# Optimization experiments

Hardware: AMD Instinct MI355X
Metric: run time of the kernel (lower is better)

The kernel has to match this reference:

```python
import jax, jax.numpy as jnp
import numpy as np

HIDDEN = 1024
SEQ = 32768


def setup_inputs() -> dict:
    key = jax.random.key(0)
    k1, k2, k3, k4 = jax.random.split(key, 4)
    scale = 1.0 / np.sqrt(HIDDEN)
    return {
        "hidden": jax.random.normal(k1, (HIDDEN,), dtype=jnp.float32),
        "encoder_outputs": jax.random.normal(k2, (SEQ, HIDDEN), dtype=jnp.float32),
        "W": jax.random.normal(k3, (HIDDEN, HIDDEN), dtype=jnp.float32) * scale,
        "b": jax.random.normal(k4, (HIDDEN,), dtype=jnp.float32) * scale,
    }


def reference(hidden, encoder_outputs, W, b):
    # method == 'general': energy_i = Linear(enc_i); score_i = hidden . energy_i
    # Batched: energies = (enc @ W.T + b) @ hidden   -> [S]
    proj = jnp.einsum("sh,oh->so", encoder_outputs, W) + b  # [S, H]
    energies = proj @ hidden                                  # [S]
    attn = jax.nn.softmax(energies, axis=-1)                  # softmax over seq
    return attn[None, None, :]                                # [1, 1, S]
```

## Files before the change

### kernel.cpp

```cpp
#include <hip/hip_runtime.h>
#include <math.h>

#define H 1024
#define S 32768

__global__ void matvec_partial_kernel(const float* __restrict__ W,
                                      const float* __restrict__ hidden,
                                      float* __restrict__ vpart) {
    const int t = threadIdx.x;
    const int b = blockIdx.x;
    const int h4 = t * 4;
    float4 acc = make_float4(0.f, 0.f, 0.f, 0.f);
    const int o0 = b * 16;
#pragma unroll
    for (int i = 0; i < 16; ++i) {
        const int o = o0 + i;
        const float hv = hidden[o];
        const float4 w = *reinterpret_cast<const float4*>(&W[(size_t)o * H + h4]);
        acc.x += hv * w.x;
        acc.y += hv * w.y;
        acc.z += hv * w.z;
        acc.w += hv * w.w;
    }
    *reinterpret_cast<float4*>(&vpart[(size_t)b * H + h4]) = acc;
}

__global__ void matvec_reduce_kernel(const float* __restrict__ vpart,
                                     float* __restrict__ v) {
    const int t = threadIdx.x;
    const int h4 = t * 4;
    float4 acc = make_float4(0.f, 0.f, 0.f, 0.f);
#pragma unroll 8
    for (int b = 0; b < 64; ++b) {
        const float4 p = *reinterpret_cast<const float4*>(&vpart[(size_t)b * H + h4]);
        acc.x += p.x;
        acc.y += p.y;
        acc.z += p.z;
        acc.w += p.w;
    }
    *reinterpret_cast<float4*>(&v[h4]) = acc;
}

__global__ void energies_kernel(const float* __restrict__ enc,
                                const float* __restrict__ v,
                                float* __restrict__ energies) {
    const int wave = threadIdx.x >> 6;
    const int lane = threadIdx.x & 63;
    const int s = blockIdx.x * 4 + wave;
    const float* row = enc + (size_t)s * H;
    float acc = 0.f;
#pragma unroll
    for (int j = 0; j < 4; ++j) {
        const int idx = j * 256 + lane * 4;
        const float4 e  = *reinterpret_cast<const float4*>(&row[idx]);
        const float4 vv = *reinterpret_cast<const float4*>(&v[idx]);
        acc += e.x * vv.x + e.y * vv.y + e.z * vv.z + e.w * vv.w;
    }
#pragma unroll
    for (int off = 32; off > 0; off >>= 1)
        acc += __shfl_down(acc, off, 64);
    if (lane == 0) energies[s] = acc;
}

__global__ void softmax_kernel(const float* __restrict__ energies,
                               float* __restrict__ out) {
    __shared__ float red[16];
    const int t = threadIdx.x;
    const int lane = t & 63;
    const int wid = t >> 6;

    float m = -INFINITY;
    for (int i = t; i < S; i += 1024) m = fmaxf(m, energies[i]);
#pragma unroll
    for (int off = 32; off > 0; off >>= 1)
        m = fmaxf(m, __shfl_down(m, off, 64));
    if (lane == 0) red[wid] = m;
    __syncthreads();
    if (t < 16) {
        float mm = red[t];
#pragma unroll
        for (int off = 8; off > 0; off >>= 1)
            mm = fmaxf(mm, __shfl_down(mm, off, 16));
        if (t == 0) red[0] = mm;
    }
    __syncthreads();
    m = red[0];
    __syncthreads();

    float ssum = 0.f;
    for (int i = t; i < S; i += 1024) ssum += __expf(energies[i] - m);
#pragma unroll
    for (int off = 32; off > 0; off >>= 1)
        ssum += __shfl_down(ssum, off, 64);
    if (lane == 0) red[wid] = ssum;
    __syncthreads();
    if (t < 16) {
        float sm = red[t];
#pragma unroll
        for (int off = 8; off > 0; off >>= 1)
            sm += __shfl_down(sm, off, 16);
        if (t == 0) red[0] = sm;
    }
    __syncthreads();
    const float inv = 1.0f / red[0];

    for (int i = t; i < S; i += 1024)
        out[i] = __expf(energies[i] - m) * inv;
}

extern "C" void kernel_launch(void* const* d_in, const int* in_sizes, int n_in,
                              void* d_out, int out_size, void* d_ws, size_t ws_size,
                              hipStream_t stream) {
    const float* hidden = (const float*)d_in[0];
    const float* enc    = (const float*)d_in[1];
    const float* W      = (const float*)d_in[2];
    float* out = (float*)d_out;

    float* vpart    = (float*)d_ws;
    float* v        = vpart + 64 * H;
    float* energies = v + H;

    matvec_partial_kernel<<<64, 256, 0, stream>>>(W, hidden, vpart);
    matvec_reduce_kernel<<<1, 256, 0, stream>>>(vpart, v);
    energies_kernel<<<S / 4, 256, 0, stream>>>(enc, v, energies);
    softmax_kernel<<<1, 1024, 0, stream>>>(energies, out);
}
```

Baseline: 218.2 us.

## Fuse per-block online-softmax max/sum into energies kernel, 4 rows per wave

The energies kernel now has each wave compute four rows, keeping v in registers, and each block emits a partial max and rescaled exp-sum (online softmax). The single-block finalize kernel then merges 2048 partials instead of scanning all 32768 energies twice, leaving only one pass to normalize. This shrinks the serial single-block work at the cost of extra exps in the energies kernel and fewer blocks (2048) for the memory-bound scan.

```diff
diff --git a/kernel.cpp b/kernel.cpp
--- a/kernel.cpp
+++ b/kernel.cpp
@@ -43,69 +43,103 @@
 
 __global__ void energies_kernel(const float* __restrict__ enc,
                                 const float* __restrict__ v,
-                                float* __restrict__ energies) {
+                                float* __restrict__ energies,
+                                float* __restrict__ mpart,
+                                float* __restrict__ spart) {
     const int wave = threadIdx.x >> 6;
     const int lane = threadIdx.x & 63;
-    const int s = blockIdx.x * 4 + wave;
-    const float* row = enc + (size_t)s * H;
-    float acc = 0.f;
+    const int gwave = blockIdx.x * 4 + wave;
+    const int s0 = gwave * 4;
+
+    float4 vv[4];
 #pragma unroll
-    for (int j = 0; j < 4; ++j) {
-        const int idx = j * 256 + lane * 4;
-        const float4 e  = *reinterpret_cast<const float4*>(&row[idx]);
-        const float4 vv = *reinterpret_cast<const float4*>(&v[idx]);
-        acc += e.x * vv.x + e.y * vv.y + e.z * vv.z + e.w * vv.w;
+    for (int j = 0; j < 4; ++j)
+        vv[j] = *reinterpret_cast<const float4*>(&v[j * 256 + lane * 4]);
+
+    float e[4];
+#pragma unroll
+    for (int r = 0; r < 4; ++r) {
+        const float* row = enc + (size_t)(s0 + r) * H;
+        float acc = 0.f;
+#pragma unroll
+        for (int j = 0; j < 4; ++j) {
+            const float4 ev = *reinterpret_cast<const float4*>(&row[j * 256 + lane * 4]);
+            acc += ev.x * vv[j].x + ev.y * vv[j].y + ev.z * vv[j].z + ev.w * vv[j].w;
+        }
+#pragma unroll
+        for (int off = 32; off > 0; off >>= 1)
+            acc += __shfl_xor(acc, off, 64);
+        e[r] = acc;
     }
-#pragma unroll
-    for (int off = 32; off > 0; off >>= 1)
-        acc += __shfl_down(acc, off, 64);
-    if (lane == 0) energies[s] = acc;
+
+    if (lane == 0) {
+        energies[s0 + 0] = e[0];
+        energies[s0 + 1] = e[1];
+        energies[s0 + 2] = e[2];
+        energies[s0 + 3] = e[3];
+    }
+
+    const float mw = fmaxf(fmaxf(e[0], e[1]), fmaxf(e[2], e[3]));
+    const float sw = __expf(e[0] - mw) + __expf(e[1] - mw) +
+                     __expf(e[2] - mw) + __expf(e[3] - mw);
+
+    __shared__ float lm[4], ls[4];
+    if (lane == 0) { lm[wave] = mw; ls[wave] = sw; }
+    __syncthreads();
+    if (threadIdx.x == 0) {
+        const float m = fmaxf(fmaxf(lm[0], lm[1]), fmaxf(lm[2], lm[3]));
+        const float s = ls[0] * __expf(lm[0] - m) + ls[1] * __expf(lm[1] - m) +
+                        ls[2] * __expf(lm[2] - m) + ls[3] * __expf(lm[3] - m);
+        mpart[blockIdx.x] = m;
+        spart[blockIdx.x] = s;
+    }
 }
 
-__global__ void softmax_kernel(const float* __restrict__ energies,
-                               float* __restrict__ out) {
+__global__ void finalize_kernel(const float* __restrict__ energies,
+                                const float* __restrict__ mpart,
+                                const float* __restrict__ spart,
+                                float* __restrict__ out) {
     __shared__ float red[16];
+    __shared__ float gm_s, gs_s;
     const int t = threadIdx.x;
     const int lane = t & 63;
     const int wid = t >> 6;
 
-    float m = -INFINITY;
-    for (int i = t; i < S; i += 1024) m = fmaxf(m, energies[i]);
+    float m = fmaxf(mpart[t], mpart[t + 1024]);
 #pragma unroll
     for (int off = 32; off > 0; off >>= 1)
-        m = fmaxf(m, __shfl_down(m, off, 64));
+        m = fmaxf(m, __shfl_xor(m, off, 64));
     if (lane == 0) red[wid] = m;
     __syncthreads();
-    if (t < 16) {
-        float mm = red[t];
+    if (t == 0) {
+        float mm = red[0];
 #pragma unroll
-        for (int off = 8; off > 0; off >>= 1)
-            mm = fmaxf(mm, __shfl_down(mm, off, 16));
-        if (t == 0) red[0] = mm;
+        for (int i = 1; i < 16; ++i) mm = fmaxf(mm, red[i]);
+        gm_s = mm;
     }
     __syncthreads();
-    m = red[0];
-    __syncthreads();
+    const float gm = gm_s;
 
-    float ssum = 0.f;
-    for (int i = t; i < S; i += 1024) ssum += __expf(energies[i] - m);
+    float s = spart[t] * __expf(mpart[t] - gm) +
+              spart[t + 1024] * __expf(mpart[t + 1024] - gm);
 #pragma unroll
     for (int off = 32; off > 0; off >>= 1)
-        ssum += __shfl_down(ssum, off, 64);
-    if (lane == 0) red[wid] = ssum;
+        s += __shfl_xor(s, off, 64);
     __syncthreads();
-    if (t < 16) {
-        float sm = red[t];
+    if (lane == 0) red[wid] = s;
+    __syncthreads();
+    if (t == 0) {
+        float ss = 0.f;
 #pragma unroll
-        for (int off = 8; off > 0; off >>= 1)
-            sm += __shfl_down(sm, off, 16);
-        if (t == 0) red[0] = sm;
+        for (int i = 0; i < 16; ++i) ss += red[i];
+        gs_s = ss;
     }
     __syncthreads();
-    const float inv = 1.0f / red[0];
+    const float inv = 1.0f / gs_s;
 
-    for (int i = t; i < S; i += 1024)
-        out[i] = __expf(energies[i] - m) * inv;
+#pragma unroll
+    for (int k = 0; k < S / 1024; ++k)
+        out[t + k * 1024] = __expf(energies[t + k * 1024] - gm) * inv;
 }
 
 extern "C" void kernel_launch(void* const* d_in, const int* in_sizes, int n_in,
@@ -119,9 +153,11 @@
     float* vpart    = (float*)d_ws;
     float* v        = vpart + 64 * H;
     float* energies = v + H;
+    float* mpart    = energies + S;
+    float* spart    = mpart + 2048;
 
     matvec_partial_kernel<<<64, 256, 0, stream>>>(W, hidden, vpart);
     matvec_reduce_kernel<<<1, 256, 0, stream>>>(vpart, v);
-    energies_kernel<<<S / 4, 256, 0, stream>>>(enc, v, energies);
-    softmax_kernel<<<1, 1024, 0, stream>>>(energies, out);
+    energies_kernel<<<2048, 256, 0, stream>>>(enc, v, energies, mpart, spart);
+    finalize_kernel<<<1, 1024, 0, stream>>>(energies, mpart, spart, out);
 }
```

New measurement: 211.6 us. 3.0% less time.
